# Kernel tuning notes

Hardware: AMD Instinct MI355X
Metric: run time of the kernel (lower is better)

The kernel has to match this reference:

```python
import jax, jax.numpy as jnp
import numpy as np

B, S, C = 4, 2048, 1024

def setup_inputs() -> dict:
    key = jax.random.key(0)
    ks = jax.random.split(key, 9)
    lim = 1.0 / np.sqrt(C)  # torch nn.Linear default init range
    def lin_params(kw, kb):
        W = jax.random.uniform(kw, (C, C), jnp.float32, -lim, lim)
        b = jax.random.uniform(kb, (C,), jnp.float32, -lim, lim)
        return W, b
    Wq, bq = lin_params(ks[0], ks[1])
    Wk, bk = lin_params(ks[2], ks[3])
    Wv, bv = lin_params(ks[4], ks[5])
    query = jax.random.normal(ks[6], (B, S, C), jnp.float32)
    key_t = jax.random.normal(ks[7], (B, S, C), jnp.float32)
    value = jax.random.normal(ks[8], (B, S, C), jnp.float32)
    return {"query": query, "key": key_t, "value": value,
            "Wq": Wq, "bq": bq, "Wk": Wk, "bk": bk, "Wv": Wv, "bv": bv}

def reference(query, key, value, Wq, bq, Wk, bk, Wv, bv):
    # Linear projections: y = x @ W^T + b (torch Linear convention, W is [out, in])
    Q = jnp.einsum('bsc,dc->bsd', query, Wq) + bq
    K = jnp.einsum('bsc,dc->bsd', key, Wk) + bk
    V = jnp.einsum('bsc,dc->bsd', value, Wv) + bv
    scale = jnp.float32(C) ** 0.5
    scores = jnp.einsum('bqd,bkd->bqk', Q, K) / scale  # [B, S, S]
    attn = jax.nn.softmax(scores, axis=-1)
    out = jnp.einsum('bqk,bkd->bqd', attn, V)  # [B, S, C]
    return out
```

## Files before the change

kernel.cpp:

```cpp
#include <hip/hip_runtime.h>
#include <hip/hip_bf16.h>


typedef _Float16 half8 __attribute__((ext_vector_type(8)));
typedef _Float16 half4 __attribute__((ext_vector_type(4)));
typedef float f32x4 __attribute__((ext_vector_type(4)));

#define AS1(p) ((const __attribute__((address_space(1))) void*)(p))
#define AS3(p) ((__attribute__((address_space(3))) void*)(p))

__global__ __launch_bounds__(256) void cvt3_f32_f16(
    const float* __restrict__ s0, const float* __restrict__ s1,
    const float* __restrict__ s2, _Float16* __restrict__ d0,
    _Float16* __restrict__ d1, _Float16* __restrict__ d2, int n) {
    const float* s = blockIdx.y == 0 ? s0 : blockIdx.y == 1 ? s1 : s2;
    _Float16* d = blockIdx.y == 0 ? d0 : blockIdx.y == 1 ? d1 : d2;
    int i = (blockIdx.x * 256 + threadIdx.x) * 8;
    if (i >= n) return;
    float4 a = *(const float4*)(s + i);
    float4 b = *(const float4*)(s + i + 4);
    half8 h;
    h[0] = (_Float16)a.x; h[1] = (_Float16)a.y; h[2] = (_Float16)a.z; h[3] = (_Float16)a.w;
    h[4] = (_Float16)b.x; h[5] = (_Float16)b.y; h[6] = (_Float16)b.z; h[7] = (_Float16)b.w;
    *(half8*)(d + i) = h;
}

template <int K, int NX_SH, int R, int NYT_SH, bool BIAS, bool F16OUT, bool PROJ3>
__global__ __launch_bounds__(256, 2)
void gemm_nt(const _Float16* __restrict__ A, const _Float16* __restrict__ Bt,
             const float* __restrict__ b0, const float* __restrict__ b1,
             const float* __restrict__ b2, void* __restrict__ Cout,
             _Float16* __restrict__ VtOut, int N, float scale,
             long sA, long sB, long sC) {
    __shared__ _Float16 Asm[128 * 64] __attribute__((aligned(16)));
    __shared__ _Float16 Bsm[128 * 64] __attribute__((aligned(16)));
    const int tid = threadIdx.x;
    const int lane = tid & 63;
    const int wave = tid >> 6;

    const int lin = blockIdx.x;
    const int g = lin & 7;
    const int s = lin >> 3;
    const int xt = s & ((1 << NX_SH) - 1);
    const int row_id = g * R + (s >> NX_SH);
    const int yt = row_id & ((1 << NYT_SH) - 1);
    const int tz = row_id >> NYT_SH;
    const int m0 = yt * 128;
    const int n0 = xt * 128;

    const float* bias = nullptr;
    if constexpr (PROJ3) {
        A += (long)tz * 8388608;
        Bt += (long)tz * 1048576;
        bias = tz == 0 ? b0 : tz == 1 ? b1 : b2;
    } else {
        A += (long)tz * sA;
        Bt += (long)tz * sB;
    }

    const int srow8 = lane >> 3;
    const int sq = ((lane & 7) ^ srow8) << 3;
    const int quad = lane >> 4;
    const int l16 = lane & 15;
    const int wm = (wave >> 1) << 6;
    const int wn = (wave & 1) << 6;
    const int fa0 = (wm + l16) * 64 + (((0 * 4 + quad) ^ (l16 & 7)) << 3);
    const int fa1 = (wm + l16) * 64 + (((1 * 4 + quad) ^ (l16 & 7)) << 3);
    const int fb0 = (wn + l16) * 64 + (((0 * 4 + quad) ^ (l16 & 7)) << 3);
    const int fb1 = (wn + l16) * 64 + (((1 * 4 + quad) ^ (l16 & 7)) << 3);

    f32x4 acc[4][4];
#pragma unroll
    for (int i = 0; i < 4; i++)
#pragma unroll
        for (int j = 0; j < 4; j++)
#pragma unroll
            for (int r = 0; r < 4; r++) acc[i][j][r] = 0.0f;

    const _Float16* Abase = A + (long)m0 * K;
    const _Float16* Bbase = Bt + (long)n0 * K;

    for (int k0 = 0; k0 < K; k0 += 64) {
        __syncthreads();
#pragma unroll
        for (int u = 0; u < 8; ++u) {
            const int t = wave + u * 4;
            if (t < 16) {
                __builtin_amdgcn_global_load_lds(
                    AS1(Abase + (long)(t * 8 + srow8) * K + k0 + sq),
                    AS3(Asm + t * 512), 16, 0, 0);
            } else {
                __builtin_amdgcn_global_load_lds(
                    AS1(Bbase + (long)((t - 16) * 8 + srow8) * K + k0 + sq),
                    AS3(Bsm + (t - 16) * 512), 16, 0, 0);
            }
        }
        __syncthreads();

#pragma unroll
        for (int ks = 0; ks < 2; ++ks) {
            const int ao = ks ? fa1 : fa0;
            const int bo = ks ? fb1 : fb0;
            half8 af[4], bf[4];
#pragma unroll
            for (int i = 0; i < 4; i++) af[i] = *(const half8*)(Asm + ao + i * 1024);
#pragma unroll
            for (int j = 0; j < 4; j++) bf[j] = *(const half8*)(Bsm + bo + j * 1024);
#pragma unroll
            for (int i = 0; i < 4; i++)
#pragma unroll
                for (int j = 0; j < 4; j++)
                    acc[i][j] = __builtin_amdgcn_mfma_f32_16x16x32_f16(af[i], bf[j], acc[i][j], 0, 0, 0);
        }
    }

    const bool trout = PROJ3 && tz == 2;
#pragma unroll
    for (int i = 0; i < 4; i++) {
        const int row = m0 + wm + i * 16 + quad * 4;
#pragma unroll
        for (int j = 0; j < 4; j++) {
            const int col = n0 + wn + j * 16 + l16;
            const float badd = BIAS ? bias[col] : 0.0f;
            if (trout) {
                const long b = row >> 11;
                const int sl = row & 2047;
                half4 h;
#pragma unroll
                for (int r = 0; r < 4; r++) h[r] = (_Float16)(acc[i][j][r] * scale + badd);
                *(half4*)(VtOut + b * 2097152 + (long)col * 2048 + sl) = h;
            } else if constexpr (PROJ3) {
                _Float16* o = (_Float16*)Cout + (long)tz * 8388608;
#pragma unroll
                for (int r = 0; r < 4; r++)
                    o[(long)(row + r) * N + col] = (_Float16)(acc[i][j][r] * scale + badd);
            } else {
#pragma unroll
                for (int r = 0; r < 4; r++) {
                    float v = acc[i][j][r] * scale + badd;
                    if constexpr (F16OUT)
                        ((_Float16*)Cout + (long)tz * sC)[(long)(row + r) * N + col] = (_Float16)v;
                    else
                        ((float*)Cout + (long)tz * sC)[(long)(row + r) * N + col] = v;
                }
            }
        }
    }
}

__global__ __launch_bounds__(256) void softmax_f16(const _Float16* __restrict__ S,
                                                   _Float16* __restrict__ P) {
    const long row = blockIdx.x;
    const int t = threadIdx.x;
    const int wave = t >> 6, lane = t & 63;
    half8 h = ((const half8*)(S + row * 2048))[t];
    float v[8];
#pragma unroll
    for (int j = 0; j < 8; j++) v[j] = (float)h[j];
    float m = v[0];
#pragma unroll
    for (int j = 1; j < 8; j++) m = fmaxf(m, v[j]);
#pragma unroll
    for (int off = 32; off > 0; off >>= 1) m = fmaxf(m, __shfl_xor(m, off, 64));
    __shared__ float redm[4], reds[4];
    if (lane == 0) redm[wave] = m;
    __syncthreads();
    m = fmaxf(fmaxf(redm[0], redm[1]), fmaxf(redm[2], redm[3]));
    float sum = 0.0f;
#pragma unroll
    for (int j = 0; j < 8; j++) { v[j] = __expf(v[j] - m); sum += v[j]; }
#pragma unroll
    for (int off = 32; off > 0; off >>= 1) sum += __shfl_xor(sum, off, 64);
    if (lane == 0) reds[wave] = sum;
    __syncthreads();
    sum = (reds[0] + reds[1]) + (reds[2] + reds[3]);
    const float inv = 1.0f / sum;
    half8 o;
#pragma unroll
    for (int j = 0; j < 8; j++) o[j] = (_Float16)(v[j] * inv);
    ((half8*)(P + row * 2048))[t] = o;
}

extern "C" void kernel_launch(void* const* d_in, const int* in_sizes, int n_in,
                              void* d_out, int out_size, void* d_ws, size_t ws_size,
                              hipStream_t stream) {
    constexpr int B = 4, S = 2048, C = 1024;
    constexpr long XSZ = (long)B * S * C;
    constexpr long WSZ = (long)C * C;

    const float* query = (const float*)d_in[0];
    const float* key   = (const float*)d_in[1];
    const float* value = (const float*)d_in[2];
    const float* Wq = (const float*)d_in[3];
    const float* bq = (const float*)d_in[4];
    const float* Wk = (const float*)d_in[5];
    const float* bk = (const float*)d_in[6];
    const float* Wv = (const float*)d_in[7];
    const float* bv = (const float*)d_in[8];
    float* out = (float*)d_out;
    char* ws = (char*)d_ws;

    _Float16* Xq  = (_Float16*)(ws + 0);
    _Float16* Wqh = (_Float16*)(ws + 3 * XSZ * 2);
    _Float16* scores = (_Float16*)(ws + 0);
    _Float16* Qh  = (_Float16*)(ws + 73400320);
    _Float16* attn = (_Float16*)(ws + 73400320);
    _Float16* Vt  = (_Float16*)(ws + 106954752);
    if (ws_size < 123731968) return;

    cvt3_f32_f16<<<dim3(XSZ / 2048, 3), 256, 0, stream>>>(
        query, key, value, Xq, Xq + XSZ, Xq + 2 * XSZ, (int)XSZ);
    cvt3_f32_f16<<<dim3(WSZ / 2048, 3), 256, 0, stream>>>(
        Wq, Wk, Wv, Wqh, Wqh + WSZ, Wqh + 2 * WSZ, (int)WSZ);

    gemm_nt<1024, 3, 24, 6, true, true, true><<<1536, 256, 0, stream>>>(
        Xq, Wqh, bq, bk, bv, Qh, Vt, C, 1.0f, 0, 0, 0);

    gemm_nt<1024, 4, 8, 4, false, true, false><<<1024, 256, 0, stream>>>(
        Qh, Qh + XSZ, nullptr, nullptr, nullptr, scores, nullptr, S, 0.03125f,
        (long)S * C, (long)S * C, (long)S * S);

    softmax_f16<<<B * S, 256, 0, stream>>>(scores, attn);

    gemm_nt<2048, 3, 8, 4, false, false, false><<<512, 256, 0, stream>>>(
        attn, Vt, nullptr, nullptr, nullptr, out, nullptr, C, 1.0f,
        (long)S * S, (long)C * S, (long)S * C);
}
```

Before: 308.6 us.

## Add 256x256 double-buffered 8-wave GEMM for projection and score GEMMs

Adds a gemm256 kernel with 256x256 output tiles and 512 threads. It double-buffers LDS and splits each K-step into four phases that interleave global->LDS prefetch of the next tile with MFMA work, using explicit waitcnt, barriers and setprio. The QKV projection and QK^T score GEMMs now use it, which raises arithmetic intensity and hides load latency. The PV GEMM still uses the old kernel. The 128KB of LDS per block combined with launch_bounds(512,2) risks low occupancy, and with only 256 to 384 blocks the tail can be poorly balanced.

```diff
diff --git a/kernel.cpp b/kernel.cpp
--- a/kernel.cpp
+++ b/kernel.cpp
@@ -8,6 +8,7 @@
 
 #define AS1(p) ((const __attribute__((address_space(1))) void*)(p))
 #define AS3(p) ((__attribute__((address_space(3))) void*)(p))
+#define MFMA16(a, b, c) __builtin_amdgcn_mfma_f32_16x16x32_f16(a, b, c, 0, 0, 0)
 
 __global__ __launch_bounds__(256) void cvt3_f32_f16(
     const float* __restrict__ s0, const float* __restrict__ s1,
@@ -110,7 +111,7 @@
             for (int i = 0; i < 4; i++)
 #pragma unroll
                 for (int j = 0; j < 4; j++)
-                    acc[i][j] = __builtin_amdgcn_mfma_f32_16x16x32_f16(af[i], bf[j], acc[i][j], 0, 0, 0);
+                    acc[i][j] = MFMA16(af[i], bf[j], acc[i][j]);
         }
     }
 
@@ -121,6 +122,206 @@
 #pragma unroll
         for (int j = 0; j < 4; j++) {
             const int col = n0 + wn + j * 16 + l16;
+            const float badd = BIAS ? bias[col] : 0.0f;
+            if (trout) {
+                const long b = row >> 11;
+                const int sl = row & 2047;
+                half4 h;
+#pragma unroll
+                for (int r = 0; r < 4; r++) h[r] = (_Float16)(acc[i][j][r] * scale + badd);
+                *(half4*)(VtOut + b * 2097152 + (long)col * 2048 + sl) = h;
+            } else if constexpr (PROJ3) {
+                _Float16* o = (_Float16*)Cout + (long)tz * 8388608;
+#pragma unroll
+                for (int r = 0; r < 4; r++)
+                    o[(long)(row + r) * N + col] = (_Float16)(acc[i][j][r] * scale + badd);
+            } else {
+#pragma unroll
+                for (int r = 0; r < 4; r++) {
+                    float v = acc[i][j][r] * scale + badd;
+                    if constexpr (F16OUT)
+                        ((_Float16*)Cout + (long)tz * sC)[(long)(row + r) * N + col] = (_Float16)v;
+                    else
+                        ((float*)Cout + (long)tz * sC)[(long)(row + r) * N + col] = v;
+                }
+            }
+        }
+    }
+}
+
+template <int K, int NX_SH, int R, int NYT_SH, bool BIAS, bool F16OUT, bool PROJ3>
+__global__ __launch_bounds__(512, 2)
+void gemm256(const _Float16* __restrict__ A, const _Float16* __restrict__ Bt,
+             const float* __restrict__ b0, const float* __restrict__ b1,
+             const float* __restrict__ b2, void* __restrict__ Cout,
+             _Float16* __restrict__ VtOut, int N, float scale,
+             long sA, long sB, long sC) {
+    constexpr int NT = K / 64;
+    static_assert(NT >= 2, "need >=2 K-tiles");
+    __shared__ _Float16 sm[2][2][256 * 64] __attribute__((aligned(16)));
+
+    const int tid = threadIdx.x;
+    const int lane = tid & 63;
+    const int wave = tid >> 6;
+    const int wm_i = wave >> 2;
+    const int wn_i = wave & 3;
+
+    const int lin = blockIdx.x;
+    const int g = lin & 7;
+    const int sblk = lin >> 3;
+    const int xt = sblk & ((1 << NX_SH) - 1);
+    const int row_id = g * R + (sblk >> NX_SH);
+    const int yt = row_id & ((1 << NYT_SH) - 1);
+    const int tz = row_id >> NYT_SH;
+    const int m0 = yt * 256;
+    const int n0 = xt * 256;
+
+    const float* bias = nullptr;
+    if constexpr (PROJ3) {
+        A += (long)tz * 8388608;
+        Bt += (long)tz * 1048576;
+        bias = tz == 0 ? b0 : tz == 1 ? b1 : b2;
+    } else {
+        A += (long)tz * sA;
+        Bt += (long)tz * sB;
+    }
+    const _Float16* Abase = A + (long)m0 * K;
+    const _Float16* Bbase = Bt + (long)n0 * K;
+
+    const int srow8 = lane >> 3;
+    const int sq = ((lane & 7) ^ srow8) << 3;
+    const int quad = lane >> 4;
+    const int l16 = lane & 15;
+    const int e7 = l16 & 7;
+    const int ch0 = (quad ^ e7) << 3;
+    const int ch1 = ((4 + quad) ^ e7) << 3;
+    const int arow = (wm_i * 128 + l16) * 64;
+    const int brow = (wn_i * 64 + l16) * 64;
+
+    f32x4 acc[8][4];
+#pragma unroll
+    for (int i = 0; i < 8; i++)
+#pragma unroll
+        for (int j = 0; j < 4; j++)
+#pragma unroll
+            for (int r = 0; r < 4; r++) acc[i][j][r] = 0.0f;
+
+    auto STAGE = [&](int bfi, int ab, int half, int kt) {
+        const _Float16* gb = ab ? Bbase : Abase;
+#pragma unroll
+        for (int u = 0; u < 2; ++u) {
+            const int c8 = (u << 3) + wave;
+            const int r = half * 128 + c8 * 8 + srow8;
+            __builtin_amdgcn_global_load_lds(
+                AS1(gb + (long)r * K + kt * 64 + sq),
+                AS3(&sm[bfi][ab][half * 8192 + c8 * 512]), 16, 0, 0);
+        }
+    };
+
+    STAGE(0, 0, 0, 0);
+    STAGE(0, 0, 1, 0);
+    STAGE(0, 1, 0, 0);
+    STAGE(0, 1, 1, 0);
+    STAGE(1, 1, 0, 1);
+    STAGE(1, 1, 1, 1);
+    asm volatile("s_waitcnt vmcnt(4)" ::: "memory");
+    __builtin_amdgcn_s_barrier();
+
+    half8 af[4][2], bfr[4][2];
+#pragma unroll 2
+    for (int t = 0; t < NT; ++t) {
+        const int c = t & 1;
+        const int nb = c ^ 1;
+        const _Float16* sAp = sm[c][0];
+        const _Float16* sBp = sm[c][1];
+
+#pragma unroll
+        for (int i = 0; i < 4; ++i) {
+            af[i][0] = *(const half8*)(sAp + arow + i * 1024 + ch0);
+            af[i][1] = *(const half8*)(sAp + arow + i * 1024 + ch1);
+        }
+#pragma unroll
+        for (int j = 0; j < 2; ++j) {
+            bfr[j][0] = *(const half8*)(sBp + brow + j * 1024 + ch0);
+            bfr[j][1] = *(const half8*)(sBp + brow + j * 1024 + ch1);
+        }
+        if (t + 1 < NT) STAGE(nb, 0, 0, t + 1);
+        __builtin_amdgcn_s_barrier();
+        asm volatile("s_waitcnt lgkmcnt(0)" ::: "memory");
+        __builtin_amdgcn_s_setprio(1);
+#pragma unroll
+        for (int i = 0; i < 4; ++i)
+#pragma unroll
+            for (int j = 0; j < 2; ++j) {
+                acc[i][j] = MFMA16(af[i][0], bfr[j][0], acc[i][j]);
+                acc[i][j] = MFMA16(af[i][1], bfr[j][1], acc[i][j]);
+            }
+        __builtin_amdgcn_s_setprio(0);
+        __builtin_amdgcn_s_barrier();
+
+#pragma unroll
+        for (int j = 2; j < 4; ++j) {
+            bfr[j][0] = *(const half8*)(sBp + brow + j * 1024 + ch0);
+            bfr[j][1] = *(const half8*)(sBp + brow + j * 1024 + ch1);
+        }
+        if (t + 1 < NT) STAGE(nb, 0, 1, t + 1);
+        __builtin_amdgcn_s_barrier();
+        asm volatile("s_waitcnt lgkmcnt(0)" ::: "memory");
+        __builtin_amdgcn_s_setprio(1);
+#pragma unroll
+        for (int i = 0; i < 4; ++i)
+#pragma unroll
+            for (int j = 2; j < 4; ++j) {
+                acc[i][j] = MFMA16(af[i][0], bfr[j][0], acc[i][j]);
+                acc[i][j] = MFMA16(af[i][1], bfr[j][1], acc[i][j]);
+            }
+        __builtin_amdgcn_s_setprio(0);
+        __builtin_amdgcn_s_barrier();
+
+#pragma unroll
+        for (int i = 0; i < 4; ++i) {
+            af[i][0] = *(const half8*)(sAp + arow + (i + 4) * 1024 + ch0);
+            af[i][1] = *(const half8*)(sAp + arow + (i + 4) * 1024 + ch1);
+        }
+        if (t + 2 < NT) STAGE(c, 1, 0, t + 2);
+        __builtin_amdgcn_s_barrier();
+        asm volatile("s_waitcnt lgkmcnt(0)" ::: "memory");
+        __builtin_amdgcn_s_setprio(1);
+#pragma unroll
+        for (int i = 0; i < 4; ++i)
+#pragma unroll
+            for (int j = 0; j < 2; ++j) {
+                acc[i + 4][j] = MFMA16(af[i][0], bfr[j][0], acc[i + 4][j]);
+                acc[i + 4][j] = MFMA16(af[i][1], bfr[j][1], acc[i + 4][j]);
+            }
+        __builtin_amdgcn_s_setprio(0);
+        __builtin_amdgcn_s_barrier();
+
+        if (t + 2 < NT) STAGE(c, 1, 1, t + 2);
+        __builtin_amdgcn_s_barrier();
+        __builtin_amdgcn_s_setprio(1);
+#pragma unroll
+        for (int i = 0; i < 4; ++i)
+#pragma unroll
+            for (int j = 2; j < 4; ++j) {
+                acc[i + 4][j] = MFMA16(af[i][0], bfr[j][0], acc[i + 4][j]);
+                acc[i + 4][j] = MFMA16(af[i][1], bfr[j][1], acc[i + 4][j]);
+            }
+        __builtin_amdgcn_s_setprio(0);
+        if (t + 2 < NT)
+            asm volatile("s_waitcnt vmcnt(4)" ::: "memory");
+        else
+            asm volatile("s_waitcnt vmcnt(0)" ::: "memory");
+        __builtin_amdgcn_s_barrier();
+    }
+
+    const bool trout = PROJ3 && tz == 2;
+#pragma unroll
+    for (int i = 0; i < 8; ++i) {
+        const int row = m0 + wm_i * 128 + i * 16 + quad * 4;
+#pragma unroll
+        for (int j = 0; j < 4; ++j) {
+            const int col = n0 + wn_i * 64 + j * 16 + l16;
             const float badd = BIAS ? bias[col] : 0.0f;
             if (trout) {
                 const long b = row >> 11;
@@ -213,10 +414,10 @@
     cvt3_f32_f16<<<dim3(WSZ / 2048, 3), 256, 0, stream>>>(
         Wq, Wk, Wv, Wqh, Wqh + WSZ, Wqh + 2 * WSZ, (int)WSZ);
 
-    gemm_nt<1024, 3, 24, 6, true, true, true><<<1536, 256, 0, stream>>>(
+    gemm256<1024, 2, 12, 5, true, true, true><<<384, 512, 0, stream>>>(
         Xq, Wqh, bq, bk, bv, Qh, Vt, C, 1.0f, 0, 0, 0);
 
-    gemm_nt<1024, 4, 8, 4, false, true, false><<<1024, 256, 0, stream>>>(
+    gemm256<1024, 3, 4, 3, false, true, false><<<256, 512, 0, stream>>>(
         Qh, Qh + XSZ, nullptr, nullptr, nullptr, scores, nullptr, S, 0.03125f,
         (long)S * C, (long)S * C, (long)S * S);
 
```

After: 320.4 us. 1.04x slower.

## Double GEMM K-tile to 128 with new LDS swizzle and merge conversion launches

Applied to the files above, without the earlier changes.

The GEMM K-step grows from 64 to 128, so each tile does twice the MFMA work per pair of barriers. This needs a new 16-chunk XOR swizzle for the LDS layout and 64 KB of shared memory per block. The larger footprint may limit how many blocks fit per CU and cut latency hiding, since loads are still not double-buffered. The two fp32-to-fp16 conversion launches are also merged into one launch, removing one kernel launch.

```diff
diff --git a/kernel.cpp b/kernel.cpp
--- a/kernel.cpp
+++ b/kernel.cpp
@@ -8,20 +8,35 @@
 
 #define AS1(p) ((const __attribute__((address_space(1))) void*)(p))
 #define AS3(p) ((__attribute__((address_space(3))) void*)(p))
-
-__global__ __launch_bounds__(256) void cvt3_f32_f16(
-    const float* __restrict__ s0, const float* __restrict__ s1,
-    const float* __restrict__ s2, _Float16* __restrict__ d0,
-    _Float16* __restrict__ d1, _Float16* __restrict__ d2, int n) {
-    const float* s = blockIdx.y == 0 ? s0 : blockIdx.y == 1 ? s1 : s2;
-    _Float16* d = blockIdx.y == 0 ? d0 : blockIdx.y == 1 ? d1 : d2;
-    int i = (blockIdx.x * 256 + threadIdx.x) * 8;
-    if (i >= n) return;
+#define MFMA16(a, b, c) __builtin_amdgcn_mfma_f32_16x16x32_f16(a, b, c, 0, 0, 0)
+
+__global__ __launch_bounds__(256) void cvt6_f32_f16(
+    const float* __restrict__ q, const float* __restrict__ k,
+    const float* __restrict__ v, const float* __restrict__ wq,
+    const float* __restrict__ wk, const float* __restrict__ wv,
+    _Float16* __restrict__ Xq, _Float16* __restrict__ Wqh) {
+    constexpr long XSZ = 8388608, WSZ = 1048576;
+    const int b = blockIdx.x;
+    const float* s;
+    _Float16* d;
+    long i;
+    if (b < 12288) {
+        const int tz = b >> 12;
+        s = tz == 0 ? q : tz == 1 ? k : v;
+        d = Xq + (long)tz * XSZ;
+        i = (long)(b & 4095) * 2048 + threadIdx.x * 8;
+    } else {
+        const int b2 = b - 12288;
+        const int tz = b2 >> 9;
+        s = tz == 0 ? wq : tz == 1 ? wk : wv;
+        d = Wqh + (long)tz * WSZ;
+        i = (long)(b2 & 511) * 2048 + threadIdx.x * 8;
+    }
     float4 a = *(const float4*)(s + i);
-    float4 b = *(const float4*)(s + i + 4);
+    float4 c = *(const float4*)(s + i + 4);
     half8 h;
     h[0] = (_Float16)a.x; h[1] = (_Float16)a.y; h[2] = (_Float16)a.z; h[3] = (_Float16)a.w;
-    h[4] = (_Float16)b.x; h[5] = (_Float16)b.y; h[6] = (_Float16)b.z; h[7] = (_Float16)b.w;
+    h[4] = (_Float16)c.x; h[5] = (_Float16)c.y; h[6] = (_Float16)c.z; h[7] = (_Float16)c.w;
     *(half8*)(d + i) = h;
 }
 
@@ -32,8 +47,8 @@
              const float* __restrict__ b2, void* __restrict__ Cout,
              _Float16* __restrict__ VtOut, int N, float scale,
              long sA, long sB, long sC) {
-    __shared__ _Float16 Asm[128 * 64] __attribute__((aligned(16)));
-    __shared__ _Float16 Bsm[128 * 64] __attribute__((aligned(16)));
+    __shared__ _Float16 Asm[128 * 128] __attribute__((aligned(16)));
+    __shared__ _Float16 Bsm[128 * 128] __attribute__((aligned(16)));
     const int tid = threadIdx.x;
     const int lane = tid & 63;
     const int wave = tid >> 6;
@@ -58,16 +73,17 @@
         Bt += (long)tz * sB;
     }
 
-    const int srow8 = lane >> 3;
-    const int sq = ((lane & 7) ^ srow8) << 3;
+    const int rin = lane >> 4;
+    const int pch = lane & 15;
     const int quad = lane >> 4;
     const int l16 = lane & 15;
     const int wm = (wave >> 1) << 6;
     const int wn = (wave & 1) << 6;
-    const int fa0 = (wm + l16) * 64 + (((0 * 4 + quad) ^ (l16 & 7)) << 3);
-    const int fa1 = (wm + l16) * 64 + (((1 * 4 + quad) ^ (l16 & 7)) << 3);
-    const int fb0 = (wn + l16) * 64 + (((0 * 4 + quad) ^ (l16 & 7)) << 3);
-    const int fb1 = (wn + l16) * 64 + (((1 * 4 + quad) ^ (l16 & 7)) << 3);
+    const int fa_base = (wm + l16) * 128;
+    const int fb_base = (wn + l16) * 128;
+    int ch[4];
+#pragma unroll
+    for (int ks = 0; ks < 4; ++ks) ch[ks] = (((ks * 4 + quad) ^ l16) << 3);
 
     f32x4 acc[4][4];
 #pragma unroll
@@ -80,37 +96,38 @@
     const _Float16* Abase = A + (long)m0 * K;
     const _Float16* Bbase = Bt + (long)n0 * K;
 
-    for (int k0 = 0; k0 < K; k0 += 64) {
+    for (int k0 = 0; k0 < K; k0 += 128) {
         __syncthreads();
 #pragma unroll
-        for (int u = 0; u < 8; ++u) {
+        for (int u = 0; u < 16; ++u) {
             const int t = wave + u * 4;
-            if (t < 16) {
+            const int sl = t & 31;
+            const int r = sl * 4 + rin;
+            const int lq = (pch ^ (((sl & 3) << 2) + rin)) << 3;
+            if (t < 32) {
                 __builtin_amdgcn_global_load_lds(
-                    AS1(Abase + (long)(t * 8 + srow8) * K + k0 + sq),
-                    AS3(Asm + t * 512), 16, 0, 0);
+                    AS1(Abase + (long)r * K + k0 + lq),
+                    AS3(Asm + sl * 512), 16, 0, 0);
             } else {
                 __builtin_amdgcn_global_load_lds(
-                    AS1(Bbase + (long)((t - 16) * 8 + srow8) * K + k0 + sq),
-                    AS3(Bsm + (t - 16) * 512), 16, 0, 0);
+                    AS1(Bbase + (long)r * K + k0 + lq),
+                    AS3(Bsm + sl * 512), 16, 0, 0);
             }
         }
         __syncthreads();
 
 #pragma unroll
-        for (int ks = 0; ks < 2; ++ks) {
-            const int ao = ks ? fa1 : fa0;
-            const int bo = ks ? fb1 : fb0;
+        for (int ks = 0; ks < 4; ++ks) {
             half8 af[4], bf[4];
 #pragma unroll
-            for (int i = 0; i < 4; i++) af[i] = *(const half8*)(Asm + ao + i * 1024);
-#pragma unroll
-            for (int j = 0; j < 4; j++) bf[j] = *(const half8*)(Bsm + bo + j * 1024);
+            for (int i = 0; i < 4; i++) af[i] = *(const half8*)(Asm + fa_base + i * 2048 + ch[ks]);
+#pragma unroll
+            for (int j = 0; j < 4; j++) bf[j] = *(const half8*)(Bsm + fb_base + j * 2048 + ch[ks]);
 #pragma unroll
             for (int i = 0; i < 4; i++)
 #pragma unroll
                 for (int j = 0; j < 4; j++)
-                    acc[i][j] = __builtin_amdgcn_mfma_f32_16x16x32_f16(af[i], bf[j], acc[i][j], 0, 0, 0);
+                    acc[i][j] = MFMA16(af[i], bf[j], acc[i][j]);
         }
     }
 
@@ -208,10 +225,8 @@
     _Float16* Vt  = (_Float16*)(ws + 106954752);
     if (ws_size < 123731968) return;
 
-    cvt3_f32_f16<<<dim3(XSZ / 2048, 3), 256, 0, stream>>>(
-        query, key, value, Xq, Xq + XSZ, Xq + 2 * XSZ, (int)XSZ);
-    cvt3_f32_f16<<<dim3(WSZ / 2048, 3), 256, 0, stream>>>(
-        Wq, Wk, Wv, Wqh, Wqh + WSZ, Wqh + 2 * WSZ, (int)WSZ);
+    cvt6_f32_f16<<<13824, 256, 0, stream>>>(
+        query, key, value, Wq, Wk, Wv, Xq, Wqh);
 
     gemm_nt<1024, 3, 24, 6, true, true, true><<<1536, 256, 0, stream>>>(
         Xq, Wqh, bq, bk, bv, Qh, Vt, C, 1.0f, 0, 0, 0);
```

New measurement: 298.2 us. 1.04x faster.
